# Kernel optimization log

Hardware: AMD Instinct MI355X
Metric: run time of the kernel (lower is better)

Reference implementation:

```python
import jax, jax.numpy as jnp
import numpy as np

D_MODEL = 1024
H = 16
D_K = D_MODEL // H


def setup_inputs() -> dict:
    key = jax.random.key(0)
    ks = jax.random.split(key, 13)
    B, S = 4, 2048
    scale = 1.0 / np.sqrt(D_MODEL)
    inp = {
        "query": jax.random.normal(ks[0], (B, S, D_MODEL), jnp.float32),
        "key": jax.random.normal(ks[1], (B, S, D_MODEL), jnp.float32),
        "value": jax.random.normal(ks[2], (B, S, D_MODEL), jnp.float32),
        "mask": jax.random.randint(ks[3], (B, S, S), 0, 2, jnp.int32),
        "Wq": jax.random.normal(ks[4], (D_MODEL, D_MODEL), jnp.float32) * scale,
        "bq": jnp.zeros((D_MODEL,), jnp.float32),
        "Wk": jax.random.normal(ks[5], (D_MODEL, D_MODEL), jnp.float32) * scale,
        "bk": jnp.zeros((D_MODEL,), jnp.float32),
        "Wv": jax.random.normal(ks[6], (D_MODEL, D_MODEL), jnp.float32) * scale,
        "bv": jnp.zeros((D_MODEL,), jnp.float32),
        "Wo": jax.random.normal(ks[7], (D_MODEL, D_MODEL), jnp.float32) * scale,
        "bo": jnp.zeros((D_MODEL,), jnp.float32),
    }
    return inp


def _split_heads(x):
    # [B, S, D] -> [B, H, S, d_k]
    B, S, _ = x.shape
    return x.reshape(B, S, H, D_K).transpose(0, 2, 1, 3)


def reference(query, key, value, mask, Wq, bq, Wk, bk, Wv, bv, Wo, bo):
    B, S, _ = query.shape
    q = _split_heads(query @ Wq + bq)
    k = _split_heads(key @ Wk + bk)
    v = _split_heads(value @ Wv + bv)
    # scores: [B, H, S, S]
    scores = jnp.einsum("bhqd,bhkd->bhqk", q, k) / jnp.sqrt(jnp.float32(D_K))
    scores = jnp.where(mask[:, None, :, :] == 0, jnp.float32(-1e9), scores)
    prob = jax.nn.softmax(scores, axis=-1)
    out = jnp.einsum("bhqk,bhkd->bhqd", prob, v)
    out = out.transpose(0, 2, 1, 3).reshape(B, S, D_MODEL)
    return out @ Wo + bo
```

## Files before the change

### kernel.cpp

```cpp
#include <hip/hip_runtime.h>
#include <hip/hip_bf16.h>


typedef __bf16 bf16;
typedef __bf16 bf16x4 __attribute__((ext_vector_type(4)));
typedef __bf16 bf16x8 __attribute__((ext_vector_type(8)));
typedef float f32x4 __attribute__((ext_vector_type(4)));
typedef float f32x16 __attribute__((ext_vector_type(16)));
typedef unsigned int uint;

__device__ __forceinline__ void gload_lds16(const void* g, void* l) {
  __builtin_amdgcn_global_load_lds(
      (__attribute__((address_space(1))) void*)g,
      (__attribute__((address_space(3))) void*)l, 16, 0, 0);
}

__global__ __launch_bounds__(256) void wt_kernel(const float* __restrict__ Wq,
                                                 const float* __restrict__ Wk,
                                                 const float* __restrict__ Wv,
                                                 const float* __restrict__ Wo,
                                                 bf16* __restrict__ wt) {
  __shared__ float tile[64][65];
  const int z = blockIdx.z;
  const float* W = (z == 0) ? Wq : (z == 1) ? Wk : (z == 2) ? Wv : Wo;
  bf16* out = wt + (size_t)z * 1048576;
  const int k0 = blockIdx.x * 64, n0 = blockIdx.y * 64;
  for (int e = threadIdx.x; e < 4096; e += 256) {
    int r = e >> 6, c = e & 63;
    tile[r][c] = W[(size_t)(k0 + r) * 1024 + n0 + c];
  }
  __syncthreads();
  for (int e = threadIdx.x; e < 4096; e += 256) {
    int r = e >> 6, c = e & 63;
    out[(size_t)(n0 + r) * 1024 + k0 + c] = (bf16)tile[c][r];
  }
}

__global__ __launch_bounds__(256) void maskpack_kernel(const int* __restrict__ mask,
                                                       unsigned long long* __restrict__ bits) {
  const int lane = threadIdx.x & 63;
  const int wv = threadIdx.x >> 6;
  const int word0 = blockIdx.x * 16 + wv * 4;
#pragma unroll
  for (int m = 0; m < 4; ++m) {
    int v = mask[(size_t)(word0 + m) * 64 + lane];
    unsigned long long b = __ballot(v != 0);
    if (lane == 0) bits[word0 + m] = b;
  }
}

__global__ __launch_bounds__(512) void qkv_gemm_kernel(
    const float* __restrict__ Aq, const float* __restrict__ Ak, const float* __restrict__ Av,
    const bf16* __restrict__ wt, const float* __restrict__ bqp, const float* __restrict__ bkp,
    const float* __restrict__ bvp, char* __restrict__ qbuf, char* __restrict__ kbuf,
    char* __restrict__ vbuf) {
  __shared__ alignas(16) char smem[32768];
  char* As = smem;
  char* Bs = smem + 16384;
  const int t = threadIdx.x;
  const int w = t >> 6, l = t & 63;
  const int hi = l >> 4, lo = l & 15, l7 = l & 7;
  const int wr = w >> 2, wc = w & 3;
  const int row0 = blockIdx.x * 128;
  const int n0 = blockIdx.y * 128;
  const int z = blockIdx.z;
  const float* A = (z == 0) ? Aq : (z == 1) ? Ak : Av;
  const char* Bb = (const char*)(wt + (size_t)z * 1048576);
  const float* bias = (z == 0) ? bqp : (z == 1) ? bkp : bvp;
  char* ob = (z == 0) ? qbuf : (z == 1) ? kbuf : vbuf;

  const f32x4 fz = {0.f, 0.f, 0.f, 0.f};
  f32x4 acc[4][2];
#pragma unroll
  for (int mi = 0; mi < 4; ++mi)
#pragma unroll
    for (int ni = 0; ni < 2; ++ni) acc[mi][ni] = fz;

  for (int kt = 0; kt < 16; ++kt) {
#pragma unroll
    for (int i = 0; i < 4; ++i) {
      int qq = i * 512 + t;
      int r = qq >> 4, q = qq & 15;
      f32x4 f = *(const f32x4*)(A + (size_t)(row0 + r) * 1024 + kt * 64 + q * 4);
      bf16x4 hq = {(bf16)f[0], (bf16)f[1], (bf16)f[2], (bf16)f[3]};
      *(bf16x4*)(As + r * 128 + ((q * 8) ^ ((r & 7) << 4))) = hq;
    }
#pragma unroll
    for (int i = 0; i < 2; ++i) {
      int c = i * 512 + t;
      int r = c >> 3, s = c & 7;
      gload_lds16(Bb + (size_t)(n0 + r) * 2048 + kt * 128 + ((s ^ (r & 7)) * 16),
                  Bs + (i * 512 + w * 64) * 16);
    }
    __syncthreads();
#pragma unroll
    for (int kk = 0; kk < 2; ++kk) {
      bf16x8 af[4], bfr[2];
#pragma unroll
      for (int mi = 0; mi < 4; ++mi)
        af[mi] = *(const bf16x8*)(As + (wr * 64 + mi * 16 + lo) * 128 +
                                  ((kk * 64 + hi * 16) ^ (l7 << 4)));
#pragma unroll
      for (int ni = 0; ni < 2; ++ni)
        bfr[ni] = *(const bf16x8*)(Bs + (wc * 32 + ni * 16 + lo) * 128 +
                                   ((kk * 64 + hi * 16) ^ (l7 << 4)));
#pragma unroll
      for (int mi = 0; mi < 4; ++mi)
#pragma unroll
        for (int ni = 0; ni < 2; ++ni)
          acc[mi][ni] =
              __builtin_amdgcn_mfma_f32_16x16x32_bf16(af[mi], bfr[ni], acc[mi][ni], 0, 0, 0);
    }
    __syncthreads();
  }

  const float scale = (z == 0) ? 0.18033688011112042f : 1.0f;
#pragma unroll
  for (int mi = 0; mi < 4; ++mi)
#pragma unroll
    for (int ni = 0; ni < 2; ++ni) {
      int gcol = n0 + wc * 32 + ni * 16 + lo;
      float bv = bias[gcol];
#pragma unroll
      for (int j = 0; j < 4; ++j) {
        int grow = row0 + wr * 64 + mi * 16 + hi * 4 + j;
        float v = (acc[mi][ni][j] + bv) * scale;
        int b = grow >> 11, si = grow & 2047, hh = gcol >> 6, d = gcol & 63;
        if (z < 2) {
          ((bf16*)ob)[((((size_t)b * 16 + hh) * 2048 + si) << 6) + d] = (bf16)v;
        } else {
          ((bf16*)ob)[((((size_t)b * 16 + hh) * 64 + d) << 11) + si] = (bf16)v;
        }
      }
    }
}

__global__ __launch_bounds__(512) void gemm3_kernel(const char* __restrict__ Aptr,
                                                    const bf16* __restrict__ Bt,
                                                    const float* __restrict__ bias,
                                                    float* __restrict__ Out) {
  __shared__ alignas(16) char smem[32768];
  char* As = smem;
  char* Bs = smem + 16384;
  const int t = threadIdx.x;
  const int w = t >> 6, l = t & 63;
  const int hi = l >> 4, lo = l & 15, l7 = l & 7;
  const int wr = w >> 2, wc = w & 3;
  const int row0 = blockIdx.x * 128;
  const int n0 = blockIdx.y * 128;

  const f32x4 fz = {0.f, 0.f, 0.f, 0.f};
  f32x4 acc[4][2];
#pragma unroll
  for (int mi = 0; mi < 4; ++mi)
#pragma unroll
    for (int ni = 0; ni < 2; ++ni) acc[mi][ni] = fz;

  for (int kt = 0; kt < 16; ++kt) {
#pragma unroll
    for (int i = 0; i < 2; ++i) {
      int c = i * 512 + t;
      int r = c >> 3, s = c & 7;
      gload_lds16(Aptr + (size_t)(row0 + r) * 2048 + kt * 128 + ((s ^ (r & 7)) * 16),
                  As + (i * 512 + w * 64) * 16);
      gload_lds16((const char*)Bt + (size_t)(n0 + r) * 2048 + kt * 128 + ((s ^ (r & 7)) * 16),
                  Bs + (i * 512 + w * 64) * 16);
    }
    __syncthreads();
#pragma unroll
    for (int kk = 0; kk < 2; ++kk) {
      bf16x8 af[4], bfr[2];
#pragma unroll
      for (int mi = 0; mi < 4; ++mi)
        af[mi] = *(const bf16x8*)(As + (wr * 64 + mi * 16 + lo) * 128 +
                                  ((kk * 64 + hi * 16) ^ (l7 << 4)));
#pragma unroll
      for (int ni = 0; ni < 2; ++ni)
        bfr[ni] = *(const bf16x8*)(Bs + (wc * 32 + ni * 16 + lo) * 128 +
                                   ((kk * 64 + hi * 16) ^ (l7 << 4)));
#pragma unroll
      for (int mi = 0; mi < 4; ++mi)
#pragma unroll
        for (int ni = 0; ni < 2; ++ni)
          acc[mi][ni] =
              __builtin_amdgcn_mfma_f32_16x16x32_bf16(af[mi], bfr[ni], acc[mi][ni], 0, 0, 0);
    }
    __syncthreads();
  }

#pragma unroll
  for (int mi = 0; mi < 4; ++mi)
#pragma unroll
    for (int ni = 0; ni < 2; ++ni) {
      int gcol = n0 + wc * 32 + ni * 16 + lo;
      float bv = bias[gcol];
#pragma unroll
      for (int j = 0; j < 4; ++j) {
        int grow = row0 + wr * 64 + mi * 16 + hi * 4 + j;
        Out[(size_t)grow * 1024 + gcol] = acc[mi][ni][j] + bv;
      }
    }
}

__global__ __launch_bounds__(512) void attn_kernel(const char* __restrict__ qb,
                                                   const char* __restrict__ kb,
                                                   const char* __restrict__ vb,
                                                   const unsigned long long* __restrict__ mbits,
                                                   bf16* __restrict__ out) {
  __shared__ alignas(16) char smem[32768];
  const int t = threadIdx.x;
  const int w = t >> 6, l = t & 63;
  const int q31 = l & 31, hi = l >> 5;
  const int bh = blockIdx.x, b = bh >> 4, h = bh & 15;
  const int q0 = blockIdx.y * 256;
  const int qrow = q0 + w * 32 + q31;

  bf16x8 qf[4];
#pragma unroll
  for (int kc = 0; kc < 4; ++kc)
    qf[kc] = *(const bf16x8*)(qb + (size_t)(bh * 2048 + qrow) * 128 + kc * 32 + hi * 16);

  const f32x16 fz16 = {0.f, 0.f, 0.f, 0.f, 0.f, 0.f, 0.f, 0.f,
                       0.f, 0.f, 0.f, 0.f, 0.f, 0.f, 0.f, 0.f};
  f32x16 o[2];
  o[0] = fz16;
  o[1] = fz16;
  float mreg = -3e38f, ls = 0.f;
  const unsigned long long* mrow = mbits + (size_t)(b * 2048 + qrow) * 32;

  for (int kt2 = 0; kt2 < 16; ++kt2) {
#pragma unroll
    for (int i = 0; i < 2; ++i) {
      int c = i * 512 + t;
      int kr = c >> 3, ks = c & 7;
      gload_lds16(kb + (size_t)(bh * 2048 + kt2 * 128 + kr) * 128 + ((ks ^ (kr & 7)) * 16),
                  smem + (i * 512 + w * 64) * 16);
      int vr = c >> 4, vs = c & 15;
      gload_lds16(vb + (size_t)(bh * 64 + vr) * 4096 + kt2 * 256 + ((vs ^ (vr & 7)) * 16),
                  smem + 16384 + (i * 512 + w * 64) * 16);
    }
    unsigned long long mw01[2] = {mrow[kt2 * 2], mrow[kt2 * 2 + 1]};
    __syncthreads();

#pragma unroll
    for (int h2 = 0; h2 < 2; ++h2) {
      const unsigned long long mw = mw01[h2];

      f32x16 sc[2];
      sc[0] = fz16;
      sc[1] = fz16;
      __builtin_amdgcn_s_setprio(1);
#pragma unroll
      for (int kc = 0; kc < 4; ++kc) {
        bf16x8 kf0 = *(const bf16x8*)(smem + (h2 * 64 + q31) * 128 +
                                      (((kc * 2 + hi) ^ (q31 & 7)) * 16));
        bf16x8 kf1 = *(const bf16x8*)(smem + (h2 * 64 + 32 + q31) * 128 +
                                      (((kc * 2 + hi) ^ (q31 & 7)) * 16));
        sc[0] = __builtin_amdgcn_mfma_f32_32x32x16_bf16(kf0, qf[kc], sc[0], 0, 0, 0);
        sc[1] = __builtin_amdgcn_mfma_f32_32x32x16_bf16(kf1, qf[kc], sc[1], 0, 0, 0);
      }
      __builtin_amdgcn_s_setprio(0);

      float sv[2][16];
      float tm = -3e38f;
#pragma unroll
      for (int n = 0; n < 2; ++n) {
        uint m32 = (uint)(mw >> (n * 32 + 4 * hi));
#pragma unroll
        for (int r = 0; r < 16; ++r) {
          const int bi = (r & 3) + 8 * (r >> 2);
          sv[n][r] = ((m32 >> bi) & 1u) ? sc[n][r] : -1e9f;
        }
#pragma unroll
        for (int r = 0; r < 16; r += 2) tm = fmaxf(fmaxf(tm, sv[n][r]), sv[n][r + 1]);
      }
      tm = fmaxf(tm, __shfl_xor(tm, 32));

      if (!__all(tm - mreg <= 4.f)) {
        float mn = fmaxf(mreg, tm);
        float scal = __builtin_amdgcn_exp2f(mreg - mn);
        ls *= scal;
        o[0] *= scal;
        o[1] *= scal;
        mreg = mn;
      }

      uint wpk[2][8];
#pragma unroll
      for (int n = 0; n < 2; ++n)
#pragma unroll
        for (int r2 = 0; r2 < 8; ++r2) {
          float p0 = __builtin_amdgcn_exp2f(sv[n][2 * r2] - mreg);
          float p1 = __builtin_amdgcn_exp2f(sv[n][2 * r2 + 1] - mreg);
          ls += p0 + p1;
          uint pk;
          asm("v_cvt_pk_bf16_f32 %0, %1, %2" : "=v"(pk) : "v"(p0), "v"(p1));
          wpk[n][r2] = pk;
        }

      __builtin_amdgcn_s_setprio(1);
#pragma unroll
      for (int n = 0; n < 2; ++n)
#pragma unroll
        for (int c2 = 0; c2 < 2; ++c2) {
          uint a0 = wpk[n][4 * c2], b0 = wpk[n][4 * c2 + 2];
          uint a1 = wpk[n][4 * c2 + 1], b1 = wpk[n][4 * c2 + 3];
          asm("v_permlane32_swap_b32 %0, %1" : "+v"(a0), "+v"(b0));
          asm("v_permlane32_swap_b32 %0, %1" : "+v"(a1), "+v"(b1));
          union {
            uint u[4];
            bf16x8 v;
          } pf;
          pf.u[0] = a0;
          pf.u[1] = a1;
          pf.u[2] = b0;
          pf.u[3] = b1;
          const int c = n * 2 + c2;
          const int slot = (h2 * 8 + c * 2 + hi);
          bf16x8 vf0 = *(const bf16x8*)(smem + 16384 + q31 * 256 +
                                        ((slot ^ (q31 & 7)) * 16));
          bf16x8 vf1 = *(const bf16x8*)(smem + 16384 + (32 + q31) * 256 +
                                        ((slot ^ (q31 & 7)) * 16));
          o[0] = __builtin_amdgcn_mfma_f32_32x32x16_bf16(vf0, pf.v, o[0], 0, 0, 0);
          o[1] = __builtin_amdgcn_mfma_f32_32x32x16_bf16(vf1, pf.v, o[1], 0, 0, 0);
        }
      __builtin_amdgcn_s_setprio(0);
    }
    __syncthreads();
  }

  ls += __shfl_xor(ls, 32);
  float inv = 1.f / ls;
  size_t rbase = (size_t)((b << 11) + qrow) * 1024 + h * 64;
#pragma unroll
  for (int db = 0; db < 2; ++db)
#pragma unroll
    for (int g = 0; g < 4; ++g) {
      bf16x4 hv = {(bf16)(o[db][4 * g] * inv), (bf16)(o[db][4 * g + 1] * inv),
                   (bf16)(o[db][4 * g + 2] * inv), (bf16)(o[db][4 * g + 3] * inv)};
      *(bf16x4*)(out + rbase + db * 32 + 8 * g + 4 * hi) = hv;
    }
}

extern "C" void kernel_launch(void* const* d_in, const int* in_sizes, int n_in,
                              void* d_out, int out_size, void* d_ws, size_t ws_size,
                              hipStream_t stream) {
  const float* query = (const float*)d_in[0];
  const float* key_ = (const float*)d_in[1];
  const float* value = (const float*)d_in[2];
  const int* mask = (const int*)d_in[3];
  const float* Wq = (const float*)d_in[4];
  const float* bq = (const float*)d_in[5];
  const float* Wk = (const float*)d_in[6];
  const float* bk = (const float*)d_in[7];
  const float* Wv = (const float*)d_in[8];
  const float* bv = (const float*)d_in[9];
  const float* Wo = (const float*)d_in[10];
  const float* bo = (const float*)d_in[11];

  char* ws = (char*)d_ws;
  bf16* wt = (bf16*)ws;
  char* qbuf = ws + 8388608;
  char* kbuf = qbuf + 16777216;
  char* vbuf = kbuf + 16777216;
  char* abuf = vbuf + 16777216;
  unsigned long long* mbits = (unsigned long long*)(abuf + 16777216);

  wt_kernel<<<dim3(16, 16, 4), 256, 0, stream>>>(Wq, Wk, Wv, Wo, wt);
  maskpack_kernel<<<16384, 256, 0, stream>>>(mask, mbits);
  qkv_gemm_kernel<<<dim3(64, 8, 3), 512, 0, stream>>>(query, key_, value, wt, bq, bk, bv,
                                                      qbuf, kbuf, vbuf);
  attn_kernel<<<dim3(64, 8), 512, 0, stream>>>(qbuf, kbuf, vbuf, mbits, (bf16*)abuf);
  gemm3_kernel<<<dim3(64, 8), 512, 0, stream>>>(abuf, wt + 3145728, bo, (float*)d_out);
}
```

Before: 279.1 us.

## Register-prefetch next tiles in QKV GEMM and attention, raise occupancy hints

```diff
diff --git a/kernel.cpp b/kernel.cpp
--- a/kernel.cpp
+++ b/kernel.cpp
@@ -49,7 +49,7 @@
   }
 }
 
-__global__ __launch_bounds__(512) void qkv_gemm_kernel(
+__global__ __launch_bounds__(512, 4) void qkv_gemm_kernel(
     const float* __restrict__ Aq, const float* __restrict__ Ak, const float* __restrict__ Av,
     const bf16* __restrict__ wt, const float* __restrict__ bqp, const float* __restrict__ bkp,
     const float* __restrict__ bvp, char* __restrict__ qbuf, char* __restrict__ kbuf,
@@ -69,6 +69,26 @@
   const float* bias = (z == 0) ? bqp : (z == 1) ? bkp : bvp;
   char* ob = (z == 0) ? qbuf : (z == 1) ? kbuf : vbuf;
 
+  int ar[4], aq_[4];
+#pragma unroll
+  for (int i = 0; i < 4; ++i) {
+    int qq = i * 512 + t;
+    ar[i] = qq >> 4;
+    aq_[i] = qq & 15;
+  }
+  auto loadA = [&](int kt, f32x4* dst) {
+#pragma unroll
+    for (int i = 0; i < 4; ++i)
+      dst[i] = *(const f32x4*)(A + (size_t)(row0 + ar[i]) * 1024 + kt * 64 + aq_[i] * 4);
+  };
+  auto writeA = [&](const f32x4* src) {
+#pragma unroll
+    for (int i = 0; i < 4; ++i) {
+      bf16x4 hq = {(bf16)src[i][0], (bf16)src[i][1], (bf16)src[i][2], (bf16)src[i][3]};
+      *(bf16x4*)(As + ar[i] * 128 + ((aq_[i] * 8) ^ ((ar[i] & 7) << 4))) = hq;
+    }
+  };
+
   const f32x4 fz = {0.f, 0.f, 0.f, 0.f};
   f32x4 acc[4][2];
 #pragma unroll
@@ -76,42 +96,48 @@
 #pragma unroll
     for (int ni = 0; ni < 2; ++ni) acc[mi][ni] = fz;
 
-  for (int kt = 0; kt < 16; ++kt) {
-#pragma unroll
-    for (int i = 0; i < 4; ++i) {
-      int qq = i * 512 + t;
-      int r = qq >> 4, q = qq & 15;
-      f32x4 f = *(const f32x4*)(A + (size_t)(row0 + r) * 1024 + kt * 64 + q * 4);
-      bf16x4 hq = {(bf16)f[0], (bf16)f[1], (bf16)f[2], (bf16)f[3]};
-      *(bf16x4*)(As + r * 128 + ((q * 8) ^ ((r & 7) << 4))) = hq;
-    }
-#pragma unroll
-    for (int i = 0; i < 2; ++i) {
-      int c = i * 512 + t;
-      int r = c >> 3, s = c & 7;
-      gload_lds16(Bb + (size_t)(n0 + r) * 2048 + kt * 128 + ((s ^ (r & 7)) * 16),
-                  Bs + (i * 512 + w * 64) * 16);
-    }
-    __syncthreads();
-#pragma unroll
-    for (int kk = 0; kk < 2; ++kk) {
-      bf16x8 af[4], bfr[2];
-#pragma unroll
-      for (int mi = 0; mi < 4; ++mi)
-        af[mi] = *(const bf16x8*)(As + (wr * 64 + mi * 16 + lo) * 128 +
-                                  ((kk * 64 + hi * 16) ^ (l7 << 4)));
-#pragma unroll
-      for (int ni = 0; ni < 2; ++ni)
-        bfr[ni] = *(const bf16x8*)(Bs + (wc * 32 + ni * 16 + lo) * 128 +
-                                   ((kk * 64 + hi * 16) ^ (l7 << 4)));
-#pragma unroll
-      for (int mi = 0; mi < 4; ++mi)
+  f32x4 aA[4], aB[4];
+  loadA(0, aA);
+  loadA(1, aB);
+
+#pragma unroll 1
+  for (int kt2 = 0; kt2 < 8; ++kt2) {
+#pragma unroll
+    for (int half = 0; half < 2; ++half) {
+      const int kt = kt2 * 2 + half;
+      writeA(half == 0 ? aA : aB);
+#pragma unroll
+      for (int i = 0; i < 2; ++i) {
+        int c = i * 512 + t;
+        int r = c >> 3, s = c & 7;
+        gload_lds16(Bb + (size_t)(n0 + r) * 2048 + kt * 128 + ((s ^ (r & 7)) * 16),
+                    Bs + (i * 512 + w * 64) * 16);
+      }
+      __syncthreads();
+      {
+        int ktn = kt + 2 > 15 ? 15 : kt + 2;
+        loadA(ktn, half == 0 ? aA : aB);
+      }
+#pragma unroll
+      for (int kk = 0; kk < 2; ++kk) {
+        bf16x8 af[4], bfr[2];
+#pragma unroll
+        for (int mi = 0; mi < 4; ++mi)
+          af[mi] = *(const bf16x8*)(As + (wr * 64 + mi * 16 + lo) * 128 +
+                                    ((kk * 64 + hi * 16) ^ (l7 << 4)));
 #pragma unroll
         for (int ni = 0; ni < 2; ++ni)
-          acc[mi][ni] =
-              __builtin_amdgcn_mfma_f32_16x16x32_bf16(af[mi], bfr[ni], acc[mi][ni], 0, 0, 0);
-    }
-    __syncthreads();
+          bfr[ni] = *(const bf16x8*)(Bs + (wc * 32 + ni * 16 + lo) * 128 +
+                                     ((kk * 64 + hi * 16) ^ (l7 << 4)));
+#pragma unroll
+        for (int mi = 0; mi < 4; ++mi)
+#pragma unroll
+          for (int ni = 0; ni < 2; ++ni)
+            acc[mi][ni] =
+                __builtin_amdgcn_mfma_f32_16x16x32_bf16(af[mi], bfr[ni], acc[mi][ni], 0, 0, 0);
+      }
+      __syncthreads();
+    }
   }
 
   const float scale = (z == 0) ? 0.18033688011112042f : 1.0f;
@@ -202,11 +228,11 @@
     }
 }
 
-__global__ __launch_bounds__(512) void attn_kernel(const char* __restrict__ qb,
-                                                   const char* __restrict__ kb,
-                                                   const char* __restrict__ vb,
-                                                   const unsigned long long* __restrict__ mbits,
-                                                   bf16* __restrict__ out) {
+__global__ __launch_bounds__(512, 4) void attn_kernel(const char* __restrict__ qb,
+                                                      const char* __restrict__ kb,
+                                                      const char* __restrict__ vb,
+                                                      const unsigned long long* __restrict__ mbits,
+                                                      bf16* __restrict__ out) {
   __shared__ alignas(16) char smem[32768];
   const int t = threadIdx.x;
   const int w = t >> 6, l = t & 63;
@@ -215,6 +241,30 @@
   const int q0 = blockIdx.y * 256;
   const int qrow = q0 + w * 32 + q31;
 
+  int kr[2], ks[2], vr[2], vs[2];
+#pragma unroll
+  for (int i = 0; i < 2; ++i) {
+    int c = i * 512 + t;
+    kr[i] = c >> 3;
+    ks[i] = c & 7;
+    vr[i] = c >> 4;
+    vs[i] = c & 15;
+  }
+  auto loadKV = [&](int kt2, bf16x8* kreg, bf16x8* vreg) {
+#pragma unroll
+    for (int i = 0; i < 2; ++i) {
+      kreg[i] = *(const bf16x8*)(kb + (size_t)(bh * 2048 + kt2 * 128 + kr[i]) * 128 + ks[i] * 16);
+      vreg[i] = *(const bf16x8*)(vb + (size_t)(bh * 64 + vr[i]) * 4096 + kt2 * 256 + vs[i] * 16);
+    }
+  };
+  auto writeKV = [&](const bf16x8* kreg, const bf16x8* vreg) {
+#pragma unroll
+    for (int i = 0; i < 2; ++i) {
+      *(bf16x8*)(smem + kr[i] * 128 + ((ks[i] ^ (kr[i] & 7)) * 16)) = kreg[i];
+      *(bf16x8*)(smem + 16384 + vr[i] * 256 + ((vs[i] ^ (vr[i] & 7)) * 16)) = vreg[i];
+    }
+  };
+
   bf16x8 qf[4];
 #pragma unroll
   for (int kc = 0; kc < 4; ++kc)
@@ -228,19 +278,15 @@
   float mreg = -3e38f, ls = 0.f;
   const unsigned long long* mrow = mbits + (size_t)(b * 2048 + qrow) * 32;
 
+  bf16x8 kreg[2], vreg[2];
+  loadKV(0, kreg, vreg);
+
+#pragma unroll 1
   for (int kt2 = 0; kt2 < 16; ++kt2) {
-#pragma unroll
-    for (int i = 0; i < 2; ++i) {
-      int c = i * 512 + t;
-      int kr = c >> 3, ks = c & 7;
-      gload_lds16(kb + (size_t)(bh * 2048 + kt2 * 128 + kr) * 128 + ((ks ^ (kr & 7)) * 16),
-                  smem + (i * 512 + w * 64) * 16);
-      int vr = c >> 4, vs = c & 15;
-      gload_lds16(vb + (size_t)(bh * 64 + vr) * 4096 + kt2 * 256 + ((vs ^ (vr & 7)) * 16),
-                  smem + 16384 + (i * 512 + w * 64) * 16);
-    }
+    writeKV(kreg, vreg);
     unsigned long long mw01[2] = {mrow[kt2 * 2], mrow[kt2 * 2 + 1]};
     __syncthreads();
+    loadKV(kt2 + 1 > 15 ? 15 : kt2 + 1, kreg, vreg);
 
 #pragma unroll
     for (int h2 = 0; h2 < 2; ++h2) {
@@ -261,7 +307,6 @@
       }
       __builtin_amdgcn_s_setprio(0);
 
-      float sv[2][16];
       float tm = -3e38f;
 #pragma unroll
       for (int n = 0; n < 2; ++n) {
@@ -269,10 +314,10 @@
 #pragma unroll
         for (int r = 0; r < 16; ++r) {
           const int bi = (r & 3) + 8 * (r >> 2);
-          sv[n][r] = ((m32 >> bi) & 1u) ? sc[n][r] : -1e9f;
+          sc[n][r] = ((m32 >> bi) & 1u) ? sc[n][r] : -1e9f;
         }
 #pragma unroll
-        for (int r = 0; r < 16; r += 2) tm = fmaxf(fmaxf(tm, sv[n][r]), sv[n][r + 1]);
+        for (int r = 0; r < 16; r += 2) tm = fmaxf(fmaxf(tm, sc[n][r]), sc[n][r + 1]);
       }
       tm = fmaxf(tm, __shfl_xor(tm, 32));
 
@@ -290,8 +335,8 @@
       for (int n = 0; n < 2; ++n)
 #pragma unroll
         for (int r2 = 0; r2 < 8; ++r2) {
-          float p0 = __builtin_amdgcn_exp2f(sv[n][2 * r2] - mreg);
-          float p1 = __builtin_amdgcn_exp2f(sv[n][2 * r2 + 1] - mreg);
+          float p0 = __builtin_amdgcn_exp2f(sc[n][2 * r2] - mreg);
+          float p1 = __builtin_amdgcn_exp2f(sc[n][2 * r2 + 1] - mreg);
           ls += p0 + p1;
           uint pk;
           asm("v_cvt_pk_bf16_f32 %0, %1, %2" : "=v"(pk) : "v"(p0), "v"(p1));
```

New measurement: 297.2 us. 6.5% more time.
